# Optimization experiments

Measured on AMD Instinct MI355X. Metric: run time of the kernel, lower is better.

The kernel has to match this reference:

```python
import jax, jax.numpy as jnp
import numpy as np


def setup_inputs() -> dict:
    key = jax.random.key(0)
    ks = jax.random.split(key, 12)
    B, T, S, D, A, E, L, V = 32, 64, 64, 1024, 512, 256, 1024, 12000
    s = 0.02  # weight scale for numerical stability
    return {
        "targets": jax.random.randint(ks[0], (B, T), 0, V),
        "options": jax.random.normal(ks[1], (B, S, D), jnp.float32),
        "h0": jax.random.normal(ks[2], (B, L), jnp.float32),
        "c0": jnp.zeros((B, L), jnp.float32),
        "emb": jax.random.normal(ks[3], (V, E), jnp.float32) * s,
        "W1": jax.random.normal(ks[4], (L, A), jnp.float32) * s,
        "b1": jnp.zeros((A,), jnp.float32),
        "W2": jax.random.normal(ks[5], (D, A), jnp.float32) * s,
        "b2": jnp.zeros((A,), jnp.float32),
        "Va": jax.random.normal(ks[6], (A, 1), jnp.float32) * s,
        "bVa": jnp.zeros((1,), jnp.float32),
        "Wx": jax.random.normal(ks[7], (D + E, 4 * L), jnp.float32) * s,
        "Wh": jax.random.normal(ks[8], (L, 4 * L), jnp.float32) * s,
        "bl": jnp.zeros((4 * L,), jnp.float32),
        "Wd": jax.random.normal(ks[9], (L, V), jnp.float32) * s,
        "bd": jnp.zeros((V,), jnp.float32),
    }


def reference(targets, options, h0, c0, emb, W1, b1, W2, b2, Va, bVa,
              Wx, Wh, bl, Wd, bd):
    L = h0.shape[-1]
    # W2(options) is step-invariant: hoist out of recurrent loop. [B,S,A]
    opt_proj = jnp.einsum('bsd,da->bsa', options, W2) + b2

    def step(carry, x_ids):
        h, c = carry
        # Bahdanau attention: score = V(tanh(W1(h) + W2(options)))
        score = jnp.tanh(h @ W1 + b1)[:, None, :] + opt_proj        # [B,S,A]
        score = jnp.einsum('bsa,ao->bso', score, Va) + bVa          # [B,S,1]
        w = jax.nn.softmax(score, axis=1)                           # [B,S,1]
        context = jnp.sum(w * options, axis=1)                      # [B,D]
        x = jnp.concatenate([context, emb[x_ids]], axis=-1)         # [B,D+E]
        # Keras LSTM cell, gate order i, f, g, o
        z = x @ Wx + h @ Wh + bl                                    # [B,4L]
        i, f, g, o = jnp.split(z, 4, axis=-1)
        c = jax.nn.sigmoid(f) * c + jax.nn.sigmoid(i) * jnp.tanh(g)
        h = jax.nn.sigmoid(o) * jnp.tanh(c)
        probs = jax.nn.softmax(h @ Wd + bd, axis=-1)                # [B,V]
        return (h, c), (probs, w[..., 0])

    (h, c), (out, attn) = jax.lax.scan(step, (h0, c0), targets.T)
    output = jnp.transpose(out, (1, 0, 2))   # [B,T,V]
    attention = attn[-1][..., None]          # last-step attention weights [B,S,1]
    return output, h, c, attention
```

## Files before the change

kernel.cpp:

```cpp
#include <hip/hip_runtime.h>
#include <math.h>


typedef _Float16 fp16;
typedef __attribute__((ext_vector_type(8))) _Float16 fp16x8;
typedef __attribute__((ext_vector_type(4))) float f32x4;

constexpr int B = 32, T = 64, S = 64, D = 1024, A = 512, E = 256, L = 1024, V = 12000;
constexpr int G = 4096;
constexpr size_t N_PROBS = (size_t)B * T * V;

__device__ inline void load_lds16(const void* g, void* l) {
  __builtin_amdgcn_global_load_lds(
      (const __attribute__((address_space(1))) unsigned int*)g,
      (__attribute__((address_space(3))) unsigned int*)l, 16, 0, 0);
}


__global__ void k_v2(const float* __restrict__ W2, const float* __restrict__ Va,
                     float* __restrict__ v2) {
  int gw = (blockIdx.x * blockDim.x + threadIdx.x) >> 6;
  int lane = threadIdx.x & 63;
  if (gw >= D) return;
  float acc = 0.f;
  for (int a = lane; a < A; a += 64) acc += W2[(size_t)gw * A + a] * Va[a];
  #pragma unroll
  for (int off = 32; off; off >>= 1) acc += __shfl_down(acc, off);
  if (lane == 0) v2[gw] = acc;
}

__global__ void k_score(const float* __restrict__ options, const float* __restrict__ v2,
                        float* __restrict__ w) {
  int row = (blockIdx.x * blockDim.x + threadIdx.x) >> 6;
  int lane = threadIdx.x & 63;
  if (row >= B * S) return;
  const float* orow = options + (size_t)row * D;
  float acc = 0.f;
  for (int d = lane; d < D; d += 64) acc += orow[d] * v2[d];
  #pragma unroll
  for (int off = 32; off; off >>= 1) acc += __shfl_down(acc, off);
  if (lane == 0) w[row] = acc;
}

__global__ __launch_bounds__(256) void k_attnctx(
    const float* __restrict__ options, const float* __restrict__ wat,
    float* __restrict__ oattn, float* __restrict__ ctx) {
  __shared__ float sw[64];
  const int b = blockIdx.x, tid = threadIdx.x;
  if (tid < 64) {
    float v = wat[b * 64 + tid];
    float m = v;
    #pragma unroll
    for (int off = 32; off; off >>= 1) m = fmaxf(m, __shfl_xor(m, off));
    float e = expf(v - m);
    float s = e;
    #pragma unroll
    for (int off = 32; off; off >>= 1) s += __shfl_xor(s, off);
    float res = e / s;
    sw[tid] = res;
    oattn[b * 64 + tid] = res;
  }
  __syncthreads();
  for (int d = tid; d < D; d += 256) {
    float acc = 0.f;
    #pragma unroll 8
    for (int s = 0; s < 64; ++s)
      acc += sw[s] * options[((size_t)(b * 64 + s)) * D + d];
    ctx[b * D + d] = acc;
  }
}

__global__ __launch_bounds__(256) void k_cx_part(
    const float* __restrict__ ctx, const float* __restrict__ Wx,
    float* __restrict__ cxp) {
  const int jt = blockIdx.x & 15;
  const int bg = (blockIdx.x >> 4) & 3;
  const int kc = blockIdx.x >> 6;
  const int j = jt * 256 + threadIdx.x;
  const int b0 = bg * 8, d0 = kc * 128;
  float acc[8];
  #pragma unroll
  for (int bb = 0; bb < 8; ++bb) acc[bb] = 0.f;
  for (int d = 0; d < 128; ++d) {
    float wv = Wx[(size_t)(d0 + d) * G + j];
    #pragma unroll
    for (int bb = 0; bb < 8; ++bb)
      acc[bb] = fmaf(ctx[(b0 + bb) * D + d0 + d], wv, acc[bb]);
  }
  #pragma unroll
  for (int bb = 0; bb < 8; ++bb)
    cxp[((size_t)kc * 32 + b0 + bb) * G + j] = acc[bb];
}

__global__ void k_cx_reduce(const float* __restrict__ cxp, const float* __restrict__ bl,
                            float* __restrict__ cx) {
  int i = blockIdx.x * 256 + threadIdx.x;
  float s = bl[i & 4095];
  #pragma unroll
  for (int kc = 0; kc < 8; ++kc) s += cxp[(size_t)kc * 131072 + i];
  cx[i] = s;
}


__global__ void k_eg(const int* __restrict__ targets, const float* __restrict__ emb,
                     fp16* __restrict__ eg) {
  int r = blockIdx.x, e = threadIdx.x;
  int tok = targets[r];
  eg[(size_t)r * E + e] = (fp16)emb[(size_t)tok * E + e];
}

__global__ __launch_bounds__(256) void k_wx2t(const float* __restrict__ Wx,
                                              fp16* __restrict__ t16) {
  __shared__ float s[64][65];
  const int et = blockIdx.x >> 6, jt = blockIdx.x & 63;
  const int e0 = et * 64, j0 = jt * 64;
  const int tid = threadIdx.x;
  const int jj = tid & 63;
  #pragma unroll
  for (int k = 0; k < 16; ++k) {
    int ee = k * 4 + (tid >> 6);
    s[ee][jj] = Wx[(size_t)(D + e0 + ee) * G + j0 + jj];
  }
  __syncthreads();
  const int jc = tid >> 2, eq = tid & 3;
  fp16x8 o0, o1;
  #pragma unroll
  for (int i = 0; i < 8; ++i) {
    o0[i] = (fp16)s[eq * 16 + i][jc];
    o1[i] = (fp16)s[eq * 16 + 8 + i][jc];
  }
  size_t dst = (size_t)(j0 + jc) * E + e0 + eq * 16;
  *(fp16x8*)(t16 + dst) = o0;
  *(fp16x8*)(t16 + dst + 8) = o1;
}

__global__ __launch_bounds__(256) void k_whp(const float* __restrict__ Wh,
                                             fp16* __restrict__ p) {
  __shared__ float s[64][65];
  const int lt = blockIdx.x & 15, ct = blockIdx.x >> 4;
  const int l0 = lt * 64, c0 = ct * 64;
  const int tid = threadIdx.x;
  const int cc = tid & 63;
  #pragma unroll
  for (int k = 0; k < 16; ++k) {
    int ll = k * 4 + (tid >> 6);
    s[ll][cc] = Wh[(size_t)(l0 + ll) * G + c0 + cc];
  }
  __syncthreads();
  const int c = tid >> 2, lq = tid & 3;
  const int col = c0 + c, g = col >> 10, jj = col & 1023;
  const int rowp = ((jj >> 2) << 4) + (g << 2) + (jj & 3);
  fp16x8 o0, o1;
  #pragma unroll
  for (int i = 0; i < 8; ++i) {
    o0[i] = (fp16)s[lq * 16 + i][c];
    o1[i] = (fp16)s[lq * 16 + 8 + i][c];
  }
  size_t dst = (size_t)rowp * L + l0 + lq * 16;
  *(fp16x8*)(p + dst) = o0;
  *(fp16x8*)(p + dst + 8) = o1;
}

__global__ void k_h0split(const float* __restrict__ h0, const float* __restrict__ c0,
                          fp16* __restrict__ h16, float* __restrict__ cst) {
  int i = blockIdx.x * 256 + threadIdx.x;
  h16[i] = (fp16)h0[i];
  cst[i] = c0[i];
}

__global__ __launch_bounds__(256) void k_pre_mfma(
    const fp16* __restrict__ Ag, const fp16* __restrict__ Bg,
    const float* __restrict__ cx, fp16* __restrict__ prep) {
  __shared__ __align__(16) char lds[32768];
  char* sA = lds;
  char* sB = lds + 16384;
  const int bid = blockIdx.x;
  const int swz = (bid & 7) * 64 + (bid >> 3);
  const int mt = swz >> 5, nt = swz & 31;
  const int m0 = mt * 128, n0 = nt * 128;
  const int tid = threadIdx.x, w = tid >> 6, lane = tid & 63;
  const int wr = w >> 1, wc = w & 1;

  f32x4 acc[4][4];
  #pragma unroll
  for (int i = 0; i < 4; ++i)
    #pragma unroll
    for (int j = 0; j < 4; ++j) acc[i][j] = (f32x4){0.f, 0.f, 0.f, 0.f};

  int rowc[4], sloc[4];
  #pragma unroll
  for (int i = 0; i < 4; ++i) {
    int c = i * 4 + w;
    rowc[i] = c * 8 + (lane >> 3);
    sloc[i] = (lane & 7) ^ (rowc[i] & 7);
  }

  for (int kk = 0; kk < 4; ++kk) {
    if (kk) __syncthreads();
    const char* ga = (const char*)Ag + kk * 128;
    const char* gb = (const char*)Bg + kk * 128;
    #pragma unroll
    for (int i = 0; i < 4; ++i) {
      int c = i * 4 + w;
      load_lds16(ga + (size_t)(m0 + rowc[i]) * 512 + sloc[i] * 16, sA + c * 1024);
      load_lds16(gb + (size_t)(n0 + rowc[i]) * 512 + sloc[i] * 16, sB + c * 1024);
    }
    __syncthreads();
    #pragma unroll
    for (int ks = 0; ks < 2; ++ks) {
      fp16x8 av[4], bv[4];
      #pragma unroll
      for (int f = 0; f < 4; ++f) {
        int ra = wr * 64 + f * 16 + (lane & 15);
        int ca = (ks * 4 + (lane >> 4)) ^ (ra & 7);
        av[f] = *(const fp16x8*)(sA + ra * 128 + ca * 16);
        int rb = wc * 64 + f * 16 + (lane & 15);
        int cb = (ks * 4 + (lane >> 4)) ^ (rb & 7);
        bv[f] = *(const fp16x8*)(sB + rb * 128 + cb * 16);
      }
      #pragma unroll
      for (int fm = 0; fm < 4; ++fm)
        #pragma unroll
        for (int fn = 0; fn < 4; ++fn)
          acc[fm][fn] = __builtin_amdgcn_mfma_f32_16x16x32_f16(
              av[fm], bv[fn], acc[fm][fn], 0, 0, 0);
    }
  }

  const int r0o = m0 + wr * 64 + ((lane >> 4) << 2);
  const int c0o = n0 + wc * 64 + (lane & 15);
  #pragma unroll
  for (int fn = 0; fn < 4; ++fn) {
    int colg = c0o + fn * 16;
    int g = colg >> 10, jj = colg & 1023;
    int jb = jj >> 2, jo = jj & 3;
    #pragma unroll
    for (int fm = 0; fm < 4; ++fm) {
      #pragma unroll
      for (int r = 0; r < 4; ++r) {
        int row = r0o + fm * 16 + r;
        int b = row >> 6, t = row & 63;
        float v = acc[fm][fn][r] + cx[(size_t)b * G + colg];
        prep[(((size_t)t * 256 + jb) * 32 + b) * 16 + jo * 4 + g] = (fp16)v;
      }
    }
  }
}

__global__ __launch_bounds__(512) void k_step7(
    const fp16* __restrict__ Whp, const fp16* __restrict__ prep,
    const fp16* __restrict__ hin, fp16* __restrict__ hout,
    float* __restrict__ cst, fp16* __restrict__ Hb16,
    float* __restrict__ out_h, float* __restrict__ out_c, int t) {
  __shared__ f32x4 zred[16][64];
  const int jb = blockIdx.x;
  const int tid = threadIdx.x;
  const int w = tid >> 6, lane = tid & 63;
  const int fr = lane & 15, kc = lane >> 4;

  f32x4 a0 = (f32x4){0.f, 0.f, 0.f, 0.f};
  f32x4 a1 = a0;
  const fp16* bb = Whp + (size_t)(jb * 16 + fr) * 1024;
  #pragma unroll
  for (int kk = 0; kk < 4; ++kk) {
    const int k0 = (w * 4 + kk) * 32 + kc * 8;
    fp16x8 bv = *(const fp16x8*)(bb + k0);
    a0 = __builtin_amdgcn_mfma_f32_16x16x32_f16(
        *(const fp16x8*)(hin + (size_t)fr * 1024 + k0), bv, a0, 0, 0, 0);
    a1 = __builtin_amdgcn_mfma_f32_16x16x32_f16(
        *(const fp16x8*)(hin + (size_t)(16 + fr) * 1024 + k0), bv, a1, 0, 0, 0);
  }
  zred[w * 2 + 0][lane] = a0;
  zred[w * 2 + 1][lane] = a1;
  __syncthreads();

  const int b = tid >> 4, col = tid & 15;
  const int g = col >> 2, jo = col & 3;
  const int lane2 = (((b & 15) >> 2) << 4) | col;
  const int reg = b & 3, m = b >> 4;
  float z = 0.f;
  #pragma unroll
  for (int ww = 0; ww < 8; ++ww) z += zred[ww * 2 + m][lane2][reg];
  z += (float)prep[(((size_t)t * 256 + jb) * 32 + b) * 16 + jo * 4 + g];
  float act;
  if (g == 2) act = 1.f - 2.f / (1.f + __expf(2.f * z));
  else        act = 1.f / (1.f + __expf(-z));
  float x4 = __shfl_xor(act, 4);
  float za = (g & 1) ? x4 : act;
  float zb = (g & 1) ? act : x4;
  float za2 = __shfl_xor(za, 8);
  float zb2 = __shfl_xor(zb, 8);
  const bool lo = (g < 2);
  float Ai = lo ? za : za2;
  float Af = lo ? zb : zb2;
  float Ag_ = lo ? za2 : za;
  float Ao = lo ? zb2 : zb;
  if (g == 0) {
    const int gj = jb * 4 + jo;
    const int ci = b * 1024 + gj;
    float cp = cst[ci];
    float cn = Af * cp + Ai * Ag_;
    float th = 1.f - 2.f / (1.f + __expf(2.f * cn));
    float hn = Ao * th;
    cst[ci] = cn;
    hout[ci] = (fp16)hn;
    Hb16[((size_t)b * 64 + t) * 1024 + gj] = (fp16)hn;
    if (t == T - 1) {
      out_h[ci] = hn;
      out_c[ci] = cn;
    }
  }
}

__global__ __launch_bounds__(256) void k_wdt(const float* __restrict__ Wd,
                                             fp16* __restrict__ Wdt) {
  __shared__ float s[64][65];
  const int lt = blockIdx.x & 15;
  const int vt = blockIdx.x >> 4;
  const int l0 = lt * 64, v0 = vt * 64;
  const int tid = threadIdx.x;
  const int lv = tid & 63;
  #pragma unroll
  for (int k = 0; k < 16; ++k) {
    int ll = k * 4 + (tid >> 6);
    int v = v0 + lv;
    s[ll][lv] = (v < V) ? Wd[(size_t)(l0 + ll) * V + v] : 0.f;
  }
  __syncthreads();
  const int vv = tid >> 2, lq = tid & 3;
  fp16x8 o0, o1;
  #pragma unroll
  for (int j = 0; j < 8; ++j) {
    o0[j] = (fp16)s[lq * 16 + j][vv];
    o1[j] = (fp16)s[lq * 16 + 8 + j][vv];
  }
  fp16* dst = Wdt + (size_t)(v0 + vv) * 1024 + l0 + lq * 16;
  *(fp16x8*)dst = o0;
  *(fp16x8*)(dst + 8) = o1;
}

__global__ __launch_bounds__(256) void k_logits_mfma(
    const fp16* __restrict__ Ag, const fp16* __restrict__ Btg,
    const float* __restrict__ bd, float* __restrict__ out) {
  __shared__ __align__(16) char lds[32768];
  char* sA = lds;
  char* sB = lds + 16384;
  const int bid = blockIdx.x;
  const int wg = (bid & 7) * 188 + (bid >> 3);
  const int nt = wg >> 4, mt = wg & 15;
  const int m0 = mt * 128, n0 = nt * 128;
  const int tid = threadIdx.x, w = tid >> 6, lane = tid & 63;
  const int wr = w >> 1, wc = w & 1;

  f32x4 acc[4][4];
  #pragma unroll
  for (int i = 0; i < 4; ++i)
    #pragma unroll
    for (int j = 0; j < 4; ++j) acc[i][j] = (f32x4){0.f, 0.f, 0.f, 0.f};

  int rowc[4], sloc[4];
  #pragma unroll
  for (int i = 0; i < 4; ++i) {
    int c = i * 4 + w;
    rowc[i] = c * 8 + (lane >> 3);
    sloc[i] = (lane & 7) ^ (rowc[i] & 7);
  }

  for (int kk = 0; kk < 16; ++kk) {
    if (kk) __syncthreads();
    const char* ga = (const char*)Ag + kk * 128;
    const char* gb = (const char*)Btg + kk * 128;
    #pragma unroll
    for (int i = 0; i < 4; ++i) {
      int c = i * 4 + w;
      load_lds16(ga + (size_t)(m0 + rowc[i]) * 2048 + sloc[i] * 16, sA + c * 1024);
      load_lds16(gb + (size_t)(n0 + rowc[i]) * 2048 + sloc[i] * 16, sB + c * 1024);
    }
    __syncthreads();
    #pragma unroll
    for (int ks = 0; ks < 2; ++ks) {
      fp16x8 av[4], bv[4];
      #pragma unroll
      for (int f = 0; f < 4; ++f) {
        int ra = wr * 64 + f * 16 + (lane & 15);
        int ca = (ks * 4 + (lane >> 4)) ^ (ra & 7);
        av[f] = *(const fp16x8*)(sA + ra * 128 + ca * 16);
        int rb = wc * 64 + f * 16 + (lane & 15);
        int cb = (ks * 4 + (lane >> 4)) ^ (rb & 7);
        bv[f] = *(const fp16x8*)(sB + rb * 128 + cb * 16);
      }
      #pragma unroll
      for (int fm = 0; fm < 4; ++fm)
        #pragma unroll
        for (int fn = 0; fn < 4; ++fn)
          acc[fm][fn] = __builtin_amdgcn_mfma_f32_16x16x32_f16(
              av[fm], bv[fn], acc[fm][fn], 0, 0, 0);
    }
  }

  float* ctile = (float*)lds;
  float bvv[4];
  #pragma unroll
  for (int fn = 0; fn < 4; ++fn) {
    int colg = n0 + wc * 64 + fn * 16 + (lane & 15);
    bvv[fn] = (colg < V) ? bd[colg] : 0.f;
  }
  #pragma unroll
  for (int p = 0; p < 2; ++p) {
    __syncthreads();
    if (wr == p) {
      const int col = wc * 64 + (lane & 15);
      #pragma unroll
      for (int fn = 0; fn < 4; ++fn) {
        #pragma unroll
        for (int fm = 0; fm < 4; ++fm) {
          int row = fm * 16 + ((lane >> 4) << 2);
          #pragma unroll
          for (int r = 0; r < 4; ++r)
            ctile[(row + r) * 128 + col + fn * 16] = acc[fm][fn][r] + bvv[fn];
        }
      }
    }
    __syncthreads();
    #pragma unroll
    for (int it = 0; it < 8; ++it) {
      int idx = it * 256 + tid;
      int row = idx >> 5, ch = idx & 31;
      int colg = n0 + ch * 4;
      if (colg < V)
        *(float4*)&out[(size_t)(m0 + p * 64 + row) * V + colg] =
            *(float4*)&ctile[row * 128 + ch * 4];
    }
  }
}

__global__ __launch_bounds__(256) void k_softmax(float* __restrict__ logits) {
  __shared__ float srow[V];
  __shared__ float sred[4];
  float* row = logits + (size_t)blockIdx.x * V;
  const int tid = threadIdx.x;
  const float4* rv = (const float4*)row;
  float4* sv = (float4*)srow;
  float m = -3.4e38f;
  for (int i = tid; i < 3000; i += 256) {
    float4 x = rv[i];
    sv[i] = x;
    m = fmaxf(fmaxf(m, fmaxf(x.x, x.y)), fmaxf(x.z, x.w));
  }
  #pragma unroll
  for (int off = 32; off; off >>= 1) m = fmaxf(m, __shfl_xor(m, off));
  if ((tid & 63) == 0) sred[tid >> 6] = m;
  __syncthreads();
  const float M = fmaxf(fmaxf(sred[0], sred[1]), fmaxf(sred[2], sred[3]));
  float s = 0.f;
  for (int i = tid; i < 3000; i += 256) {
    float4 x = sv[i];
    x.x = __expf(x.x - M); x.y = __expf(x.y - M);
    x.z = __expf(x.z - M); x.w = __expf(x.w - M);
    sv[i] = x;
    s += x.x + x.y + x.z + x.w;
  }
  #pragma unroll
  for (int off = 32; off; off >>= 1) s += __shfl_xor(s, off);
  __syncthreads();
  if ((tid & 63) == 0) sred[tid >> 6] = s;
  __syncthreads();
  const float inv = 1.f / (sred[0] + sred[1] + sred[2] + sred[3]);
  float4* ov = (float4*)row;
  for (int i = tid; i < 3000; i += 256) {
    float4 x = sv[i];
    x.x *= inv; x.y *= inv; x.z *= inv; x.w *= inv;
    ov[i] = x;
  }
}


extern "C" void kernel_launch(void* const* d_in, const int* in_sizes, int n_in,
                              void* d_out, int out_size, void* d_ws, size_t ws_size,
                              hipStream_t stream) {
  const int*   targets = (const int*)d_in[0];
  const float* options = (const float*)d_in[1];
  const float* h0      = (const float*)d_in[2];
  const float* c0      = (const float*)d_in[3];
  const float* emb     = (const float*)d_in[4];
  const float* W2      = (const float*)d_in[7];
  const float* Va      = (const float*)d_in[9];
  const float* Wx      = (const float*)d_in[11];
  const float* Wh      = (const float*)d_in[12];
  const float* bl      = (const float*)d_in[13];
  const float* Wd      = (const float*)d_in[14];
  const float* bd      = (const float*)d_in[15];

  float* out      = (float*)d_out;
  float* out_h    = out + N_PROBS;
  float* out_c    = out_h + (size_t)B * L;
  float* out_attn = out_c + (size_t)B * L;

  char* wsb = (char*)d_ws;
  float* v2     = (float*)(wsb);
  float* wat    = (float*)(wsb + 4096);
  float* ctx    = (float*)(wsb + 12288);
  float* cx     = (float*)(wsb + 143360);
  float* cst    = (float*)(wsb + 667648);
  fp16*  hA     = (fp16*)(wsb + 798720);
  fp16*  hB     = (fp16*)(wsb + 864256);
  fp16*  Eg16   = (fp16*)(wsb + 1191936);
  fp16*  Wx2t16 = (fp16*)(wsb + 2240512);
  fp16*  Hb16   = (fp16*)(wsb + 1191936);
  fp16*  Whp    = (fp16*)(wsb + 7483392);
  fp16*  prep   = (fp16*)(wsb + 15872000);
  float* cxp    = (float*)(wsb + 15872000);
  fp16*  Wdt    = (fp16*)(wsb + 7483392);

  k_v2<<<256, 256, 0, stream>>>(W2, Va, v2);
  k_score<<<512, 256, 0, stream>>>(options, v2, wat);
  k_attnctx<<<32, 256, 0, stream>>>(options, wat, out_attn, ctx);
  k_cx_part<<<512, 256, 0, stream>>>(ctx, Wx, cxp);
  k_cx_reduce<<<512, 256, 0, stream>>>(cxp, bl, cx);

  k_eg<<<2048, 256, 0, stream>>>(targets, emb, Eg16);
  k_wx2t<<<256, 256, 0, stream>>>(Wx, Wx2t16);
  k_whp<<<1024, 256, 0, stream>>>(Wh, Whp);

  k_pre_mfma<<<512, 256, 0, stream>>>(Eg16, Wx2t16, cx, prep);
  k_h0split<<<128, 256, 0, stream>>>(h0, c0, hA, cst);

  for (int t = 0; t < T; ++t) {
    const fp16* hin = (t & 1) ? hB : hA;
    fp16* hout = (t & 1) ? hA : hB;
    k_step7<<<256, 512, 0, stream>>>(Whp, prep, hin, hout, cst, Hb16,
                                     out_h, out_c, t);
  }

  k_wdt<<<188 * 16, 256, 0, stream>>>(Wd, Wdt);
  k_logits_mfma<<<1504, 256, 0, stream>>>(Hb16, Wdt, bd, out);
  k_softmax<<<B * T, 256, 0, stream>>>(out);
}
```

Before: 571.1 us.

## Split LSTM step across batch halves and keep softmax rows in registers

The recurrent step kernel now launches 512 blocks of 256 threads, each handling 16 batch rows for one gate block, instead of 256 blocks of 512 threads covering all 32 rows. Each wave accumulates over a 256-wide K slice, so the cross-wave LDS reduction shrinks from 8 partials to 4. The prep and c-state loads are also issued before the MFMA loop so their latency overlaps the matrix math. The softmax keeps each row's 12 float4 chunks in registers rather than staging the 48KB row in shared memory, which frees LDS and should raise occupancy. In exchange, the step kernel now loads each Wh tile twice, once per batch half, and the softmax uses more registers.

```diff
diff --git a/kernel.cpp b/kernel.cpp
--- a/kernel.cpp
+++ b/kernel.cpp
@@ -247,41 +247,45 @@
   }
 }
 
-__global__ __launch_bounds__(512) void k_step7(
+__global__ __launch_bounds__(256) void k_step8(
     const fp16* __restrict__ Whp, const fp16* __restrict__ prep,
     const fp16* __restrict__ hin, fp16* __restrict__ hout,
     float* __restrict__ cst, fp16* __restrict__ Hb16,
     float* __restrict__ out_h, float* __restrict__ out_c, int t) {
-  __shared__ f32x4 zred[16][64];
-  const int jb = blockIdx.x;
+  __shared__ f32x4 zred[4][64];
+  const int jb = blockIdx.x >> 1, bh = blockIdx.x & 1;
   const int tid = threadIdx.x;
   const int w = tid >> 6, lane = tid & 63;
   const int fr = lane & 15, kc = lane >> 4;
 
-  f32x4 a0 = (f32x4){0.f, 0.f, 0.f, 0.f};
-  f32x4 a1 = a0;
-  const fp16* bb = Whp + (size_t)(jb * 16 + fr) * 1024;
-  #pragma unroll
-  for (int kk = 0; kk < 4; ++kk) {
-    const int k0 = (w * 4 + kk) * 32 + kc * 8;
-    fp16x8 bv = *(const fp16x8*)(bb + k0);
+  const int b_local = tid >> 4, col = tid & 15;
+  const int b = bh * 16 + b_local;
+  const int g = col >> 2, jo = col & 3;
+  const int gj = jb * 4 + jo;
+  const float pfv = (float)prep[(((size_t)t * 256 + jb) * 32 + b) * 16 + jo * 4 + g];
+  const float cp = (g == 0) ? cst[b * 1024 + gj] : 0.f;
+
+  f32x4 a0 = (f32x4){0.f, 0.f, 0.f, 0.f}, a1 = a0;
+  const fp16* bb = Whp + (size_t)(jb * 16 + fr) * 1024 + w * 256 + kc * 8;
+  const fp16* aa = hin + (size_t)(bh * 16 + fr) * 1024 + w * 256 + kc * 8;
+  #pragma unroll
+  for (int kk = 0; kk < 8; kk += 2) {
     a0 = __builtin_amdgcn_mfma_f32_16x16x32_f16(
-        *(const fp16x8*)(hin + (size_t)fr * 1024 + k0), bv, a0, 0, 0, 0);
+        *(const fp16x8*)(aa + kk * 32), *(const fp16x8*)(bb + kk * 32), a0, 0, 0, 0);
     a1 = __builtin_amdgcn_mfma_f32_16x16x32_f16(
-        *(const fp16x8*)(hin + (size_t)(16 + fr) * 1024 + k0), bv, a1, 0, 0, 0);
-  }
-  zred[w * 2 + 0][lane] = a0;
-  zred[w * 2 + 1][lane] = a1;
-  __syncthreads();
-
-  const int b = tid >> 4, col = tid & 15;
-  const int g = col >> 2, jo = col & 3;
-  const int lane2 = (((b & 15) >> 2) << 4) | col;
-  const int reg = b & 3, m = b >> 4;
-  float z = 0.f;
-  #pragma unroll
-  for (int ww = 0; ww < 8; ++ww) z += zred[ww * 2 + m][lane2][reg];
-  z += (float)prep[(((size_t)t * 256 + jb) * 32 + b) * 16 + jo * 4 + g];
+        *(const fp16x8*)(aa + (kk + 1) * 32), *(const fp16x8*)(bb + (kk + 1) * 32), a1, 0, 0, 0);
+  }
+  f32x4 zv;
+  #pragma unroll
+  for (int q = 0; q < 4; ++q) zv[q] = a0[q] + a1[q];
+  zred[w][lane] = zv;
+  __syncthreads();
+
+  const int lane2 = ((b_local >> 2) << 4) | col;
+  const int reg = b_local & 3;
+  float z = zred[0][lane2][reg] + zred[1][lane2][reg]
+          + zred[2][lane2][reg] + zred[3][lane2][reg];
+  z += pfv;
   float act;
   if (g == 2) act = 1.f - 2.f / (1.f + __expf(2.f * z));
   else        act = 1.f / (1.f + __expf(-z));
@@ -296,9 +300,7 @@
   float Ag_ = lo ? za2 : za;
   float Ao = lo ? zb2 : zb;
   if (g == 0) {
-    const int gj = jb * 4 + jo;
     const int ci = b * 1024 + gj;
-    float cp = cst[ci];
     float cn = Af * cp + Ai * Ag_;
     float th = 1.f - 2.f / (1.f + __expf(2.f * cn));
     float hn = Ao * th;
@@ -435,17 +437,19 @@
 }
 
 __global__ __launch_bounds__(256) void k_softmax(float* __restrict__ logits) {
-  __shared__ float srow[V];
   __shared__ float sred[4];
   float* row = logits + (size_t)blockIdx.x * V;
   const int tid = threadIdx.x;
   const float4* rv = (const float4*)row;
-  float4* sv = (float4*)srow;
+  float4 v[12];
   float m = -3.4e38f;
-  for (int i = tid; i < 3000; i += 256) {
-    float4 x = rv[i];
-    sv[i] = x;
-    m = fmaxf(fmaxf(m, fmaxf(x.x, x.y)), fmaxf(x.z, x.w));
+  #pragma unroll
+  for (int k = 0; k < 12; ++k) {
+    int i = tid + k * 256;
+    if (i < 3000) {
+      v[k] = rv[i];
+      m = fmaxf(fmaxf(m, fmaxf(v[k].x, v[k].y)), fmaxf(v[k].z, v[k].w));
+    }
   }
   #pragma unroll
   for (int off = 32; off; off >>= 1) m = fmaxf(m, __shfl_xor(m, off));
@@ -453,12 +457,14 @@
   __syncthreads();
   const float M = fmaxf(fmaxf(sred[0], sred[1]), fmaxf(sred[2], sred[3]));
   float s = 0.f;
-  for (int i = tid; i < 3000; i += 256) {
-    float4 x = sv[i];
-    x.x = __expf(x.x - M); x.y = __expf(x.y - M);
-    x.z = __expf(x.z - M); x.w = __expf(x.w - M);
-    sv[i] = x;
-    s += x.x + x.y + x.z + x.w;
+  #pragma unroll
+  for (int k = 0; k < 12; ++k) {
+    int i = tid + k * 256;
+    if (i < 3000) {
+      v[k].x = __expf(v[k].x - M); v[k].y = __expf(v[k].y - M);
+      v[k].z = __expf(v[k].z - M); v[k].w = __expf(v[k].w - M);
+      s += v[k].x + v[k].y + v[k].z + v[k].w;
+    }
   }
   #pragma unroll
   for (int off = 32; off; off >>= 1) s += __shfl_xor(s, off);
@@ -467,10 +473,14 @@
   __syncthreads();
   const float inv = 1.f / (sred[0] + sred[1] + sred[2] + sred[3]);
   float4* ov = (float4*)row;
-  for (int i = tid; i < 3000; i += 256) {
-    float4 x = sv[i];
-    x.x *= inv; x.y *= inv; x.z *= inv; x.w *= inv;
-    ov[i] = x;
+  #pragma unroll
+  for (int k = 0; k < 12; ++k) {
+    int i = tid + k * 256;
+    if (i < 3000) {
+      float4 x = v[k];
+      x.x *= inv; x.y *= inv; x.z *= inv; x.w *= inv;
+      ov[i] = x;
+    }
   }
 }
 
@@ -528,7 +538,7 @@
   for (int t = 0; t < T; ++t) {
     const fp16* hin = (t & 1) ? hB : hA;
     fp16* hout = (t & 1) ? hA : hB;
-    k_step7<<<256, 512, 0, stream>>>(Whp, prep, hin, hout, cst, Hb16,
+    k_step8<<<512, 256, 0, stream>>>(Whp, prep, hin, hout, cst, Hb16,
                                      out_h, out_c, t);
   }
 
```

Result: slower. 585.6 us (+2.5%).
